# Performance work log

Measured on AMD Instinct MI355X. Metric: run time of the kernel, lower is better.

## Reference

```python
import jax, jax.numpy as jnp
import numpy as np

V, E, H, L, B, S = 32000, 256, 512, 2, 128, 512


def _lstm_step(x, h, c, w_ih, w_hh, b_ih, b_hh):
    # PyTorch gate order: i, f, g, o
    gates = x @ w_ih.T + b_ih + h @ w_hh.T + b_hh
    i, f, g, o = jnp.split(gates, 4, axis=-1)
    c2 = jax.nn.sigmoid(f) * c + jax.nn.sigmoid(i) * jnp.tanh(g)
    h2 = jax.nn.sigmoid(o) * jnp.tanh(c2)
    return h2, c2


def setup_inputs() -> dict:
    key = jax.random.key(0)
    ks = jax.random.split(key, 16)
    s = 0.05
    d = {}
    d["dec_input"] = jax.random.randint(ks[0], (B,), 0, V)
    d["hidden"] = jax.random.normal(ks[1], (L, B, H), jnp.float32)
    d["cell"] = jax.random.normal(ks[2], (L, B, H), jnp.float32)
    d["encoder_outputs"] = jax.random.normal(ks[3], (S, B, H), jnp.float32)
    d["emb"] = jax.random.normal(ks[4], (V, E), jnp.float32) * s
    d["attn_w"] = jax.random.normal(ks[5], (1, 2 * H), jnp.float32) * s
    d["attn_b"] = jnp.zeros((1,), jnp.float32)
    d["w_ih0"] = jax.random.normal(ks[6], (4 * H, E + H), jnp.float32) * s
    d["w_hh0"] = jax.random.normal(ks[7], (4 * H, H), jnp.float32) * s
    d["b_ih0"] = jnp.zeros((4 * H,), jnp.float32)
    d["b_hh0"] = jnp.zeros((4 * H,), jnp.float32)
    d["w_ih1"] = jax.random.normal(ks[8], (4 * H, H), jnp.float32) * s
    d["w_hh1"] = jax.random.normal(ks[9], (4 * H, H), jnp.float32) * s
    d["b_ih1"] = jnp.zeros((4 * H,), jnp.float32)
    d["b_hh1"] = jnp.zeros((4 * H,), jnp.float32)
    d["fc_w"] = jax.random.normal(ks[10], (V, H), jnp.float32) * s
    d["fc_b"] = jnp.zeros((V,), jnp.float32)
    return d


def reference(dec_input, hidden, cell, encoder_outputs, emb, attn_w, attn_b,
              w_ih0, w_hh0, b_ih0, b_hh0, w_ih1, w_hh1, b_ih1, b_hh1,
              fc_w, fc_b):
    # embedded: [B, E]  (dropout p=0 -> identity)
    embedded = emb[dec_input]
    # Bahdanau-style additive scoring using FIRST-layer hidden (as in source)
    h0 = hidden[0]                                   # [B, H]
    w_enc, w_hid = attn_w[0, :H], attn_w[0, H:]      # split linear over concat
    # logits[b,s] = enc[s,b]@w_enc + h0[b]@w_hid + b
    logits = jnp.einsum('sbh,h->bs', encoder_outputs, w_enc) \
        + (h0 @ w_hid)[:, None] + attn_b[0]          # [B, S]
    alpha = jax.nn.softmax(logits, axis=1)           # softmax over src positions
    # context = sum_s alpha[b,s] * enc[s,b,:]  (avoids repeat_interleave blowup)
    context = jnp.einsum('bs,sbh->bh', alpha, encoder_outputs)  # [B, H]
    x = jnp.concatenate([context, embedded], axis=1)            # [B, H+E]
    # single-timestep 2-layer LSTM
    h_0, c_0 = _lstm_step(x, hidden[0], cell[0], w_ih0, w_hh0, b_ih0, b_hh0)
    h_1, c_1 = _lstm_step(h_0, hidden[1], cell[1], w_ih1, w_hh1, b_ih1, b_hh1)
    new_hidden = jnp.stack([h_0, h_1])
    new_cell = jnp.stack([c_0, c_1])
    prediction = h_1 @ fc_w.T + fc_b                 # [B, V]
    return prediction, new_hidden, new_cell
```

## Files before the change

kernel.cpp:

```cpp
#include <hip/hip_runtime.h>
#include <hip/hip_bf16.h>
#include <math.h>

constexpr int NV = 32000;
constexpr int NE = 256;
constexpr int NH = 512;
constexpr int NB = 128;
constexpr int NS = 512;
constexpr int NX = NH + NE;
constexpr int NSC = 8;

typedef __attribute__((ext_vector_type(8))) short short8;
typedef __attribute__((ext_vector_type(4))) short short4v;
typedef __attribute__((ext_vector_type(4))) float f32x4;

constexpr size_t OFF_PCTX  = 0;
constexpr size_t OFF_PML   = OFF_PCTX  + (size_t)NB*NSC*NH;
constexpr size_t OFF_XBF   = OFF_PML   + (size_t)NB*NSC*2;
constexpr size_t OFF_H0NBF = OFF_XBF   + 49152;
constexpr size_t OFF_H1NBF = OFF_H0NBF + 32768;
constexpr size_t OFF_H0BFI = OFF_H1NBF + 32768;
constexpr size_t OFF_H1BFI = OFF_H0BFI + 32768;

constexpr size_t OUT_HID  = (size_t)NB * NV;
constexpr size_t OUT_CELL = OUT_HID + 2ull * NB * NH;

__device__ inline float sigf(float x) { return 1.0f / (1.0f + expf(-x)); }
__device__ inline short bf16s(float x) {
  __hip_bfloat16 h = __float2bfloat16(x);
  return *reinterpret_cast<short*>(&h);
}

__global__ __launch_bounds__(256) void attn_partial_k(
    const float* __restrict__ enc, const float* __restrict__ attn_w,
    float* __restrict__ pctx, float* __restrict__ pml) {
  const int sc = blockIdx.x, b = blockIdx.y;
  const int wv = threadIdx.x >> 6, lane = threadIdx.x & 63;
  const f32x4 wa = *reinterpret_cast<const f32x4*>(attn_w + lane * 4);
  const f32x4 wb = *reinterpret_cast<const f32x4*>(attn_w + 256 + lane * 4);
  float m0 = -INFINITY, l0 = 0.f, m1 = -INFINITY, l1 = 0.f;
  f32x4 a00 = {}, a01 = {}, a10 = {}, a11 = {};
  const float* base = enc + ((size_t)(sc * 64 + wv) * NB + b) * NH;
  for (int i = 0; i < 8; ++i) {
    const float* r0 = base + (size_t)(i * 4) * NB * NH;
    const float* r1 = base + (size_t)((i + 8) * 4) * NB * NH;
    f32x4 e00 = *reinterpret_cast<const f32x4*>(r0 + lane * 4);
    f32x4 e01 = *reinterpret_cast<const f32x4*>(r0 + 256 + lane * 4);
    f32x4 e10 = *reinterpret_cast<const f32x4*>(r1 + lane * 4);
    f32x4 e11 = *reinterpret_cast<const f32x4*>(r1 + 256 + lane * 4);
    float d0 = e00.x * wa.x + e00.y * wa.y + e00.z * wa.z + e00.w * wa.w
             + e01.x * wb.x + e01.y * wb.y + e01.z * wb.z + e01.w * wb.w;
    float d1 = e10.x * wa.x + e10.y * wa.y + e10.z * wa.z + e10.w * wa.w
             + e11.x * wb.x + e11.y * wb.y + e11.z * wb.z + e11.w * wb.w;
#pragma unroll
    for (int off = 32; off; off >>= 1) {
      d0 += __shfl_xor(d0, off);
      d1 += __shfl_xor(d1, off);
    }
    float mn0 = fmaxf(m0, d0), mn1 = fmaxf(m1, d1);
    float s0 = expf(m0 - mn0), s1 = expf(m1 - mn1);
    float p0 = expf(d0 - mn0), p1 = expf(d1 - mn1);
    l0 = l0 * s0 + p0;         l1 = l1 * s1 + p1;
    a00 = a00 * s0 + p0 * e00; a01 = a01 * s0 + p0 * e01;
    a10 = a10 * s1 + p1 * e10; a11 = a11 * s1 + p1 * e11;
    m0 = mn0; m1 = mn1;
  }
  const float Mw = fmaxf(m0, m1);
  const float c0 = expf(m0 - Mw), c1 = expf(m1 - Mw);
  const float lw = l0 * c0 + l1 * c1;
  const f32x4 accA = a00 * c0 + a10 * c1;
  const f32x4 accB = a01 * c0 + a11 * c1;
  __shared__ float sm[4], sl[4], sacc[4][NH];
  if (lane == 0) { sm[wv] = Mw; sl[wv] = lw; }
  *reinterpret_cast<f32x4*>(&sacc[wv][lane * 4]) = accA;
  *reinterpret_cast<f32x4*>(&sacc[wv][256 + lane * 4]) = accB;
  __syncthreads();
  const float M = fmaxf(fmaxf(sm[0], sm[1]), fmaxf(sm[2], sm[3]));
  const float e0 = expf(sm[0] - M), e1 = expf(sm[1] - M),
              e2 = expf(sm[2] - M), e3 = expf(sm[3] - M);
  const int t = threadIdx.x;
  float* outc = pctx + ((size_t)b * NSC + sc) * NH;
#pragma unroll
  for (int q = 0; q < 2; ++q) {
    int h = q * 256 + t;
    outc[h] = sacc[0][h] * e0 + sacc[1][h] * e1 + sacc[2][h] * e2 + sacc[3][h] * e3;
  }
  if (t == 0) {
    pml[((size_t)b * NSC + sc) * 2 + 0] = M;
    pml[((size_t)b * NSC + sc) * 2 + 1] = sl[0] * e0 + sl[1] * e1 + sl[2] * e2 + sl[3] * e3;
  }
}

__global__ __launch_bounds__(256) void attn_finish_k(
    const float* __restrict__ pctx, const float* __restrict__ pml,
    const float* __restrict__ emb, const int* __restrict__ dec,
    const float* __restrict__ hidden,
    __hip_bfloat16* __restrict__ xbf,
    __hip_bfloat16* __restrict__ h0bf, __hip_bfloat16* __restrict__ h1bf) {
  const int b = blockIdx.x, t = threadIdx.x;
  float ms[NSC];
  float M = -INFINITY;
#pragma unroll
  for (int sc = 0; sc < NSC; ++sc) {
    ms[sc] = pml[((size_t)b * NSC + sc) * 2 + 0];
    M = fmaxf(M, ms[sc]);
  }
  float L = 0.f, es[NSC];
#pragma unroll
  for (int sc = 0; sc < NSC; ++sc) {
    es[sc] = expf(ms[sc] - M);
    L += pml[((size_t)b * NSC + sc) * 2 + 1] * es[sc];
  }
  const float invL = 1.f / L;
#pragma unroll
  for (int q = 0; q < 2; ++q) {
    int h = q * 256 + t;
    float v = 0.f;
#pragma unroll
    for (int sc = 0; sc < NSC; ++sc)
      v += pctx[((size_t)b * NSC + sc) * NH + h] * es[sc];
    xbf[(size_t)b * NX + h] = __float2bfloat16(v * invL);
    h0bf[(size_t)b * NH + h] = __float2bfloat16(hidden[(size_t)b * NH + h]);
    h1bf[(size_t)b * NH + h] =
        __float2bfloat16(hidden[(size_t)(NB * NH) + (size_t)b * NH + h]);
  }
  xbf[(size_t)b * NX + NH + t] = __float2bfloat16(emb[(size_t)dec[b] * NE + t]);
}

constexpr int LSLAB = 520;
__global__ __launch_bounds__(256, 1) void lstm_fused_k(
    const float* __restrict__ Wx, int Kx, const float* __restrict__ Wh,
    const __hip_bfloat16* __restrict__ Ax, const __hip_bfloat16* __restrict__ Ah,
    const float* __restrict__ b_ih, const float* __restrict__ b_hh,
    const float* __restrict__ c_in,
    float* __restrict__ h_out, float* __restrict__ c_out,
    __hip_bfloat16* __restrict__ hbf_out) {
  __shared__ short wlds[2][8 * LSLAB];
  __shared__ float sg[NB][17];
  const int tid = threadIdx.x, wv = tid >> 6, lane = tid & 63;
  const int l15 = lane & 15, lhi = lane >> 4;
  const int p = blockIdx.x;
  const int NCHX = Kx >> 8, NCH = NCHX + 2;
  const int srow = tid >> 6;
  const int scol = lane * 4;
  const int soff0 = (scol >> 5) * LSLAB + (scol & 31);

  f32x4 wr[4];
#define LSTAGE_LOAD(c)                                                        \
  {                                                                           \
    const bool fx = (c) < NCHX;                                               \
    const float* Ws = fx ? Wx : Wh;                                           \
    const int Ks = fx ? Kx : NH;                                              \
    const int cb = fx ? (c) * 256 : ((c) - NCHX) * 256;                       \
    _Pragma("unroll")                                                         \
    for (int i = 0; i < 4; ++i)                                               \
      wr[i] = *reinterpret_cast<const f32x4*>(                                \
          Ws + (size_t)(i * NH + p * 4 + srow) * Ks + cb + scol);             \
  }
#define LSTAGE_WRITE(buf)                                                     \
  {                                                                           \
    _Pragma("unroll")                                                         \
    for (int i = 0; i < 4; ++i) {                                             \
      short4v cv;                                                             \
      cv[0] = bf16s(wr[i].x); cv[1] = bf16s(wr[i].y);                         \
      cv[2] = bf16s(wr[i].z); cv[3] = bf16s(wr[i].w);                         \
      *reinterpret_cast<short4v*>((buf) + soff0 + (i * 4 + srow) * 32) = cv;  \
    }                                                                         \
  }

  LSTAGE_LOAD(0);
  LSTAGE_WRITE(wlds[0]);
  __syncthreads();

  f32x4 acc0 = {}, acc1 = {};
  for (int c = 0; c < NCH; ++c) {
    if (c + 1 < NCH) LSTAGE_LOAD(c + 1);
    {
      const bool fx = c < NCHX;
      const __hip_bfloat16* As = fx ? Ax : Ah;
      const int Ks = fx ? Kx : NH;
      const int cb = fx ? c * 256 : (c - NCHX) * 256;
      const short* wb = wlds[c & 1];
      const __hip_bfloat16* ar0 = As + (size_t)(wv * 32 + l15) * Ks + cb + lhi * 8;
      const __hip_bfloat16* ar1 = ar0 + (size_t)16 * Ks;
#pragma unroll
      for (int ks = 0; ks < 8; ++ks) {
        short8 bf = *reinterpret_cast<const short8*>(wb + ks * LSLAB + l15 * 32 + lhi * 8);
        short8 a0 = *reinterpret_cast<const short8*>(ar0 + ks * 32);
        short8 a1 = *reinterpret_cast<const short8*>(ar1 + ks * 32);
        acc0 = __builtin_amdgcn_mfma_f32_16x16x32_bf16(a0, bf, acc0, 0, 0, 0);
        acc1 = __builtin_amdgcn_mfma_f32_16x16x32_bf16(a1, bf, acc1, 0, 0, 0);
      }
    }
    if (c + 1 < NCH) {
      LSTAGE_WRITE(wlds[(c + 1) & 1]);
      __syncthreads();
    }
  }
#pragma unroll
  for (int q = 0; q < 4; ++q) {
    sg[wv * 32 + lhi * 4 + q][l15] = acc0[q];
    sg[wv * 32 + 16 + lhi * 4 + q][l15] = acc1[q];
  }
  __syncthreads();
#pragma unroll
  for (int it = 0; it < 2; ++it) {
    const int item = tid + it * 256;
    const int b = item >> 2, r = item & 3;
    const int h = p * 4 + r;
    float ig = sg[b][0 + r]  + b_ih[0 * NH + h] + b_hh[0 * NH + h];
    float fg = sg[b][4 + r]  + b_ih[1 * NH + h] + b_hh[1 * NH + h];
    float gg = sg[b][8 + r]  + b_ih[2 * NH + h] + b_hh[2 * NH + h];
    float og = sg[b][12 + r] + b_ih[3 * NH + h] + b_hh[3 * NH + h];
    float c = c_in[(size_t)b * NH + h];
    float c2 = sigf(fg) * c + sigf(ig) * tanhf(gg);
    float h2 = sigf(og) * tanhf(c2);
    c_out[(size_t)b * NH + h] = c2;
    h_out[(size_t)b * NH + h] = h2;
    hbf_out[(size_t)b * NH + h] = __float2bfloat16(h2);
  }
#undef LSTAGE_LOAD
#undef LSTAGE_WRITE
}

constexpr int FC_PANELS = 8;
constexpr int FC_BLOCKS = NV / (16 * FC_PANELS);
constexpr int SLAB = 520;

__global__ __launch_bounds__(256, 1) void gemm_fc_pipe_k(
    const __hip_bfloat16* __restrict__ Abf, const float* __restrict__ W,
    const float* __restrict__ bias, float* __restrict__ out) {
  __shared__ short wlds[2][16 * SLAB];
  const int tid = threadIdx.x, wv = tid >> 6, lane = tid & 63;
  const int l15 = lane & 15, lhi = lane >> 4;
  const int nbase = blockIdx.x * (16 * FC_PANELS);

  int soff[8];
#pragma unroll
  for (int i = 0; i < 8; ++i) {
    const int o = i * 1024 + tid * 4;
    const int n = o >> 9, kk = o & 511;
    soff[i] = (kk >> 5) * SLAB + n * 32 + (kk & 31);
  }

  short8 af[2][16];
#pragma unroll
  for (int m = 0; m < 2; ++m) {
    const __hip_bfloat16* ar = Abf + (size_t)(wv * 32 + m * 16 + l15) * NH + lhi * 8;
#pragma unroll
    for (int ks = 0; ks < 16; ++ks)
      af[m][ks] = *reinterpret_cast<const short8*>(ar + ks * 32);
  }

  f32x4 wr[8];
  {
    const float* panel = W + (size_t)nbase * NH;
#pragma unroll
    for (int i = 0; i < 8; ++i)
      wr[i] = *reinterpret_cast<const f32x4*>(panel + i * 1024 + tid * 4);
    short* wb0 = wlds[0];
#pragma unroll
    for (int i = 0; i < 8; ++i) {
      short4v cv;
      cv[0] = bf16s(wr[i].x); cv[1] = bf16s(wr[i].y);
      cv[2] = bf16s(wr[i].z); cv[3] = bf16s(wr[i].w);
      *reinterpret_cast<short4v*>(wb0 + soff[i]) = cv;
    }
  }
  __syncthreads();

  f32x4 s0 = {}, s1 = {};
  int sn0 = -1;
  for (int p = 0; p < FC_PANELS; ++p) {
    if (p < FC_PANELS - 1) {
      const float* panel = W + (size_t)(nbase + (p + 1) * 16) * NH;
#pragma unroll
      for (int i = 0; i < 8; ++i)
        wr[i] = *reinterpret_cast<const f32x4*>(panel + i * 1024 + tid * 4);
    }
    if (sn0 >= 0) {
      const float bv = bias[sn0 + l15];
#pragma unroll
      for (int q = 0; q < 4; ++q) {
        out[(size_t)(wv * 32 + 0 * 16 + lhi * 4 + q) * NV + sn0 + l15] = s0[q] + bv;
        out[(size_t)(wv * 32 + 1 * 16 + lhi * 4 + q) * NV + sn0 + l15] = s1[q] + bv;
      }
    }
    {
      const short* wb = wlds[p & 1];
      f32x4 a0 = {}, a1 = {};
#pragma unroll
      for (int ks = 0; ks < 16; ++ks) {
        short8 bf = *reinterpret_cast<const short8*>(wb + ks * SLAB + l15 * 32 + lhi * 8);
        a0 = __builtin_amdgcn_mfma_f32_16x16x32_bf16(af[0][ks], bf, a0, 0, 0, 0);
        a1 = __builtin_amdgcn_mfma_f32_16x16x32_bf16(af[1][ks], bf, a1, 0, 0, 0);
      }
      s0 = a0; s1 = a1; sn0 = nbase + p * 16;
    }
    if (p < FC_PANELS - 1) {
      short* wbn = wlds[(p + 1) & 1];
#pragma unroll
      for (int i = 0; i < 8; ++i) {
        short4v cv;
        cv[0] = bf16s(wr[i].x); cv[1] = bf16s(wr[i].y);
        cv[2] = bf16s(wr[i].z); cv[3] = bf16s(wr[i].w);
        *reinterpret_cast<short4v*>(wbn + soff[i]) = cv;
      }
      __syncthreads();
    }
  }
  {
    const float bv = bias[sn0 + l15];
#pragma unroll
    for (int q = 0; q < 4; ++q) {
      out[(size_t)(wv * 32 + 0 * 16 + lhi * 4 + q) * NV + sn0 + l15] = s0[q] + bv;
      out[(size_t)(wv * 32 + 1 * 16 + lhi * 4 + q) * NV + sn0 + l15] = s1[q] + bv;
    }
  }
}

extern "C" void kernel_launch(void* const* d_in, const int* in_sizes, int n_in,
                              void* d_out, int out_size, void* d_ws, size_t ws_size,
                              hipStream_t stream) {
  const int*   dec    = (const int*)d_in[0];
  const float* hidden = (const float*)d_in[1];
  const float* cell   = (const float*)d_in[2];
  const float* enc    = (const float*)d_in[3];
  const float* emb    = (const float*)d_in[4];
  const float* attn_w = (const float*)d_in[5];
  const float* w_ih0  = (const float*)d_in[7];
  const float* w_hh0  = (const float*)d_in[8];
  const float* b_ih0  = (const float*)d_in[9];
  const float* b_hh0  = (const float*)d_in[10];
  const float* w_ih1  = (const float*)d_in[11];
  const float* w_hh1  = (const float*)d_in[12];
  const float* b_ih1  = (const float*)d_in[13];
  const float* b_hh1  = (const float*)d_in[14];
  const float* fc_w   = (const float*)d_in[15];
  const float* fc_b   = (const float*)d_in[16];
  float* out = (float*)d_out;
  float* ws  = (float*)d_ws;

  float* pctx = ws + OFF_PCTX;
  float* pml  = ws + OFF_PML;
  __hip_bfloat16* xbf   = (__hip_bfloat16*)(ws + OFF_XBF);
  __hip_bfloat16* h0nbf = (__hip_bfloat16*)(ws + OFF_H0NBF);
  __hip_bfloat16* h1nbf = (__hip_bfloat16*)(ws + OFF_H1NBF);
  __hip_bfloat16* h0bf  = (__hip_bfloat16*)(ws + OFF_H0BFI);
  __hip_bfloat16* h1bf  = (__hip_bfloat16*)(ws + OFF_H1BFI);

  attn_partial_k<<<dim3(NSC, NB), 256, 0, stream>>>(enc, attn_w, pctx, pml);
  attn_finish_k<<<NB, 256, 0, stream>>>(pctx, pml, emb, dec, hidden,
                                        xbf, h0bf, h1bf);
  lstm_fused_k<<<NH / 4, 256, 0, stream>>>(w_ih0, NX, w_hh0, xbf, h0bf,
                                           b_ih0, b_hh0, cell,
                                           out + OUT_HID, out + OUT_CELL, h0nbf);
  lstm_fused_k<<<NH / 4, 256, 0, stream>>>(w_ih1, NH, w_hh1, h0nbf, h1bf,
                                           b_ih1, b_hh1, cell + NB * NH,
                                           out + OUT_HID + (size_t)NB * NH,
                                           out + OUT_CELL + (size_t)NB * NH, h1nbf);
  gemm_fc_pipe_k<<<FC_BLOCKS, 256, 0, stream>>>(h1nbf, fc_w, fc_b, out);
}
```

Baseline: 76.76 us.

## Split LSTM kernels over batch halves and preload activations into registers

The LSTM gate kernel now launches a 2D grid, with each block covering 64 batch rows instead of 128. This doubles the block count from 128 to 256 so more CUs stay busy. Each wave keeps its whole activation row slice in registers (the af array), loaded up front, instead of reading A from global memory inside the MFMA loop. K is now a template parameter so the chunk loop can fully unroll. The cost is that each weight slab is loaded and converted to bf16 twice (once per batch half), and register pressure rises, which may limit latency hiding.

```diff
diff --git a/kernel.cpp b/kernel.cpp
--- a/kernel.cpp
+++ b/kernel.cpp
@@ -128,29 +128,42 @@
 }
 
 constexpr int LSLAB = 520;
+template <int KX>
 __global__ __launch_bounds__(256, 1) void lstm_fused_k(
-    const float* __restrict__ Wx, int Kx, const float* __restrict__ Wh,
+    const float* __restrict__ Wx, const float* __restrict__ Wh,
     const __hip_bfloat16* __restrict__ Ax, const __hip_bfloat16* __restrict__ Ah,
     const float* __restrict__ b_ih, const float* __restrict__ b_hh,
     const float* __restrict__ c_in,
     float* __restrict__ h_out, float* __restrict__ c_out,
     __hip_bfloat16* __restrict__ hbf_out) {
+  constexpr int NCHX = KX / 256;
+  constexpr int NCH = NCHX + 2;
+  constexpr int NKS = NCH * 8;
   __shared__ short wlds[2][8 * LSLAB];
-  __shared__ float sg[NB][17];
+  __shared__ float sg[64][17];
   const int tid = threadIdx.x, wv = tid >> 6, lane = tid & 63;
   const int l15 = lane & 15, lhi = lane >> 4;
-  const int p = blockIdx.x;
-  const int NCHX = Kx >> 8, NCH = NCHX + 2;
+  const int p = blockIdx.x, mh = blockIdx.y;
   const int srow = tid >> 6;
   const int scol = lane * 4;
   const int soff0 = (scol >> 5) * LSLAB + (scol & 31);
+
+  const int arow = mh * 64 + wv * 16 + l15;
+  short8 af[NKS];
+#pragma unroll
+  for (int ks = 0; ks < KX / 32; ++ks)
+    af[ks] = *reinterpret_cast<const short8*>(Ax + (size_t)arow * KX + ks * 32 + lhi * 8);
+#pragma unroll
+  for (int ks = 0; ks < 16; ++ks)
+    af[KX / 32 + ks] =
+        *reinterpret_cast<const short8*>(Ah + (size_t)arow * NH + ks * 32 + lhi * 8);
 
   f32x4 wr[4];
 #define LSTAGE_LOAD(c)                                                        \
   {                                                                           \
     const bool fx = (c) < NCHX;                                               \
     const float* Ws = fx ? Wx : Wh;                                           \
-    const int Ks = fx ? Kx : NH;                                              \
+    const int Ks = fx ? KX : NH;                                              \
     const int cb = fx ? (c) * 256 : ((c) - NCHX) * 256;                       \
     _Pragma("unroll")                                                         \
     for (int i = 0; i < 4; ++i)                                               \
@@ -172,24 +185,16 @@
   LSTAGE_WRITE(wlds[0]);
   __syncthreads();
 
-  f32x4 acc0 = {}, acc1 = {};
+  f32x4 acc = {};
+#pragma unroll
   for (int c = 0; c < NCH; ++c) {
     if (c + 1 < NCH) LSTAGE_LOAD(c + 1);
     {
-      const bool fx = c < NCHX;
-      const __hip_bfloat16* As = fx ? Ax : Ah;
-      const int Ks = fx ? Kx : NH;
-      const int cb = fx ? c * 256 : (c - NCHX) * 256;
       const short* wb = wlds[c & 1];
-      const __hip_bfloat16* ar0 = As + (size_t)(wv * 32 + l15) * Ks + cb + lhi * 8;
-      const __hip_bfloat16* ar1 = ar0 + (size_t)16 * Ks;
 #pragma unroll
       for (int ks = 0; ks < 8; ++ks) {
         short8 bf = *reinterpret_cast<const short8*>(wb + ks * LSLAB + l15 * 32 + lhi * 8);
-        short8 a0 = *reinterpret_cast<const short8*>(ar0 + ks * 32);
-        short8 a1 = *reinterpret_cast<const short8*>(ar1 + ks * 32);
-        acc0 = __builtin_amdgcn_mfma_f32_16x16x32_bf16(a0, bf, acc0, 0, 0, 0);
-        acc1 = __builtin_amdgcn_mfma_f32_16x16x32_bf16(a1, bf, acc1, 0, 0, 0);
+        acc = __builtin_amdgcn_mfma_f32_16x16x32_bf16(af[c * 8 + ks], bf, acc, 0, 0, 0);
       }
     }
     if (c + 1 < NCH) {
@@ -198,20 +203,17 @@
     }
   }
 #pragma unroll
-  for (int q = 0; q < 4; ++q) {
-    sg[wv * 32 + lhi * 4 + q][l15] = acc0[q];
-    sg[wv * 32 + 16 + lhi * 4 + q][l15] = acc1[q];
-  }
+  for (int q = 0; q < 4; ++q)
+    sg[wv * 16 + lhi * 4 + q][l15] = acc[q];
   __syncthreads();
-#pragma unroll
-  for (int it = 0; it < 2; ++it) {
-    const int item = tid + it * 256;
-    const int b = item >> 2, r = item & 3;
+  {
+    const int bl = tid >> 2, r = tid & 3;
+    const int b = mh * 64 + bl;
     const int h = p * 4 + r;
-    float ig = sg[b][0 + r]  + b_ih[0 * NH + h] + b_hh[0 * NH + h];
-    float fg = sg[b][4 + r]  + b_ih[1 * NH + h] + b_hh[1 * NH + h];
-    float gg = sg[b][8 + r]  + b_ih[2 * NH + h] + b_hh[2 * NH + h];
-    float og = sg[b][12 + r] + b_ih[3 * NH + h] + b_hh[3 * NH + h];
+    float ig = sg[bl][0 + r]  + b_ih[0 * NH + h] + b_hh[0 * NH + h];
+    float fg = sg[bl][4 + r]  + b_ih[1 * NH + h] + b_hh[1 * NH + h];
+    float gg = sg[bl][8 + r]  + b_ih[2 * NH + h] + b_hh[2 * NH + h];
+    float og = sg[bl][12 + r] + b_ih[3 * NH + h] + b_hh[3 * NH + h];
     float c = c_in[(size_t)b * NH + h];
     float c2 = sigf(fg) * c + sigf(ig) * tanhf(gg);
     float h2 = sigf(og) * tanhf(c2);
@@ -352,12 +354,12 @@
   attn_partial_k<<<dim3(NSC, NB), 256, 0, stream>>>(enc, attn_w, pctx, pml);
   attn_finish_k<<<NB, 256, 0, stream>>>(pctx, pml, emb, dec, hidden,
                                         xbf, h0bf, h1bf);
-  lstm_fused_k<<<NH / 4, 256, 0, stream>>>(w_ih0, NX, w_hh0, xbf, h0bf,
-                                           b_ih0, b_hh0, cell,
-                                           out + OUT_HID, out + OUT_CELL, h0nbf);
-  lstm_fused_k<<<NH / 4, 256, 0, stream>>>(w_ih1, NH, w_hh1, h0nbf, h1bf,
-                                           b_ih1, b_hh1, cell + NB * NH,
-                                           out + OUT_HID + (size_t)NB * NH,
-                                           out + OUT_CELL + (size_t)NB * NH, h1nbf);
+  lstm_fused_k<NX><<<dim3(NH / 4, 2), 256, 0, stream>>>(
+      w_ih0, w_hh0, xbf, h0bf, b_ih0, b_hh0, cell,
+      out + OUT_HID, out + OUT_CELL, h0nbf);
+  lstm_fused_k<NH><<<dim3(NH / 4, 2), 256, 0, stream>>>(
+      w_ih1, w_hh1, h0nbf, h1bf, b_ih1, b_hh1, cell + NB * NH,
+      out + OUT_HID + (size_t)NB * NH,
+      out + OUT_CELL + (size_t)NB * NH, h1nbf);
   gemm_fc_pipe_k<<<FC_BLOCKS, 256, 0, stream>>>(h1nbf, fc_w, fc_b, out);
 }
```

Result: faster. 67.63 us (-11.9%).
